# Kernel optimization log

Hardware: AMD Instinct MI355X
Metric: run time of the kernel (lower is better)

## Reference

```python
import jax, jax.numpy as jnp
import numpy as np
import math

B, T, D, NH, HS, NB = 1024, 64, 512, 8, 64, 225  # batch, squares, d_model, heads, head_size, buckets

def _displacement_buckets():
    sq = np.arange(T)
    rank, file = sq // 8, sq % 8
    d_rank = rank[None, :] - rank[:, None]
    d_file = file[None, :] - file[:, None]
    return jnp.asarray((d_rank + 7) * 15 + (d_file + 7))  # (64, 64) in [0, 225)

BUCKET = _displacement_buckets()

def setup_inputs() -> dict:
    key = jax.random.key(0)
    ks = jax.random.split(key, 6)
    return {
        "x": jax.random.normal(ks[0], (B, T, D), dtype=jnp.float32),
        "w_qkv": jax.random.normal(ks[1], (3 * D, D), dtype=jnp.float32) * 0.02,
        "w_proj": jax.random.normal(ks[2], (D, D), dtype=jnp.float32) * 0.02,
        "b_proj": jnp.zeros((D,), dtype=jnp.float32),
        "rel_k": jax.random.normal(ks[3], (NB, HS), dtype=jnp.float32) * 0.02,
        "rel_v": jax.random.normal(ks[4], (NB, HS), dtype=jnp.float32) * 0.02,
    }

def reference(x, w_qkv, w_proj, b_proj, rel_k, rel_v):
    b, t, d = x.shape
    qkv = x @ w_qkv.T                                   # (b, t, 3d)
    qkv = qkv.reshape(b, t, 3, NH, HS)                  # 'b t (three nh h)'
    q, k, v = jnp.moveaxis(qkv, 2, 0).transpose(0, 1, 3, 2, 4)  # each (b, nh, t, h)
    scale = 1.0 / math.sqrt(HS)
    rk = rel_k[BUCKET]                                  # (t, t, h)
    rv = rel_v[BUCKET]                                  # (t, t, h)
    logits = jnp.einsum('bhid,bhjd->bhij', q, k) + jnp.einsum('bhid,ijd->bhij', q, rk)
    attn = jax.nn.softmax(logits * scale, axis=-1)      # (b, nh, t, t)
    out = jnp.einsum('bhij,bhjd->bhid', attn, v) + jnp.einsum('bhij,ijd->bhid', attn, rv)
    out = out.transpose(0, 2, 1, 3).reshape(b, t, d)    # 'b nh t h -> b t (nh h)'
    return out @ w_proj.T + b_proj
```

## Files before the change

### kernel.cpp

```cpp
#include <hip/hip_runtime.h>
#include <hip/hip_bf16.h>
#include <stdint.h>
#include <stddef.h>

typedef __attribute__((ext_vector_type(8))) short bf16x8;
typedef __attribute__((ext_vector_type(4))) float f32x4;

typedef __attribute__((address_space(1))) const unsigned int g_as1;
typedef __attribute__((address_space(3))) unsigned int lds_as3;
__device__ __forceinline__ void gload_lds16(const void* g, void* l) {
  __builtin_amdgcn_global_load_lds((g_as1*)g, (lds_as3*)l, 16, 0, 0);
}

__device__ __forceinline__ unsigned short f2bf(float f) {
  union { float f; unsigned int u; } v; v.f = f;
  unsigned int u = v.u;
  u += 0x7fffu + ((u >> 16) & 1u);
  return (unsigned short)(u >> 16);
}
__device__ __forceinline__ float bf2f(unsigned short s) {
  union { unsigned int u; float f; } v; v.u = ((unsigned int)s) << 16;
  return v.f;
}
__device__ __forceinline__ unsigned cvt_pk_bf16(float lo, float hi) {
  __hip_bfloat162 h2 = __float22bfloat162_rn(make_float2(lo, hi));
  unsigned r;
  __builtin_memcpy(&r, &h2, 4);
  return r;
}


__global__ void prep_kernel(const float* __restrict__ wqkv,
                            const float* __restrict__ wproj,
                            const float* __restrict__ relk,
                            const float* __restrict__ relv,
                            short* __restrict__ wq_t,
                            short* __restrict__ wp_t,
                            short* __restrict__ relk_b,
                            short* __restrict__ relvT_b) {
  const int g = blockIdx.x * 256 + threadIdx.x;
  if (g < 98304) {
    const int row = g >> 6, c8 = g & 63;
    const float* s = wqkv + (size_t)row * 512 + c8 * 8;
    float4 f0 = *(const float4*)s;
    float4 f1 = *(const float4*)(s + 4);
    uint4 w;
    w.x = f2bf(f0.x) | ((unsigned)f2bf(f0.y) << 16);
    w.y = f2bf(f0.z) | ((unsigned)f2bf(f0.w) << 16);
    w.z = f2bf(f1.x) | ((unsigned)f2bf(f1.y) << 16);
    w.w = f2bf(f1.z) | ((unsigned)f2bf(f1.w) << 16);
    const int bn = row >> 7, rl = row & 127, kk = c8 >> 3, c8l = c8 & 7;
    char* d = (char*)wq_t + (size_t)(bn * 8 + kk) * 16384 + rl * 128 +
              ((c8l * 16) ^ ((rl & 7) << 4));
    *(uint4*)d = w;
  } else if (g < 131072) {
    const int g2 = g - 98304;
    const int row = g2 >> 6, c8 = g2 & 63;
    const float* s = wproj + (size_t)row * 512 + c8 * 8;
    float4 f0 = *(const float4*)s;
    float4 f1 = *(const float4*)(s + 4);
    uint4 w;
    w.x = f2bf(f0.x) | ((unsigned)f2bf(f0.y) << 16);
    w.y = f2bf(f0.z) | ((unsigned)f2bf(f0.w) << 16);
    w.z = f2bf(f1.x) | ((unsigned)f2bf(f1.y) << 16);
    w.w = f2bf(f1.z) | ((unsigned)f2bf(f1.w) << 16);
    const int bn = row >> 7, rl = row & 127, kk = c8 >> 3, c8l = c8 & 7;
    char* d = (char*)wp_t + (size_t)(bn * 8 + kk) * 16384 + rl * 128 +
              ((c8l * 16) ^ ((rl & 7) << 4));
    *(uint4*)d = w;
  } else if (g < 133120) {
    const int g3 = g - 131072;
    const int nb = g3 >> 3, c8 = g3 & 7;
    uint4 w = {0u, 0u, 0u, 0u};
    if (nb < 225) {
      const float* s = relk + (size_t)nb * 64 + c8 * 8;
      float4 f0 = *(const float4*)s;
      float4 f1 = *(const float4*)(s + 4);
      w.x = f2bf(f0.x) | ((unsigned)f2bf(f0.y) << 16);
      w.y = f2bf(f0.z) | ((unsigned)f2bf(f0.w) << 16);
      w.z = f2bf(f1.x) | ((unsigned)f2bf(f1.y) << 16);
      w.w = f2bf(f1.z) | ((unsigned)f2bf(f1.w) << 16);
    }
    *(uint4*)(relk_b + nb * 64 + c8 * 8) = w;
  } else {
    const int g4 = g - 133120;
    const int d = g4 >> 5, nb0 = (g4 & 31) * 8;
    unsigned short s[8];
#pragma unroll
    for (int j = 0; j < 8; ++j) {
      const int nb = nb0 + j;
      s[j] = (nb < 225) ? f2bf(relv[(size_t)nb * 64 + d]) : (unsigned short)0;
    }
    uint4 w;
    w.x = s[0] | ((unsigned)s[1] << 16);
    w.y = s[2] | ((unsigned)s[3] << 16);
    w.z = s[4] | ((unsigned)s[5] << 16);
    w.w = s[6] | ((unsigned)s[7] << 16);
    *(uint4*)(relvT_b + d * 256 + nb0) = w;
  }
}

__global__ void xconv_kernel(const float* __restrict__ x, short* __restrict__ x_t) {
  const int g = blockIdx.x * 256 + threadIdx.x;
  const int row = g >> 6, c8 = g & 63;
  const float* s = x + (size_t)row * 512 + c8 * 8;
  float4 f0 = *(const float4*)s;
  float4 f1 = *(const float4*)(s + 4);
  uint4 w;
  w.x = f2bf(f0.x) | ((unsigned)f2bf(f0.y) << 16);
  w.y = f2bf(f0.z) | ((unsigned)f2bf(f0.w) << 16);
  w.z = f2bf(f1.x) | ((unsigned)f2bf(f1.y) << 16);
  w.w = f2bf(f1.z) | ((unsigned)f2bf(f1.w) << 16);
  const int bm = row >> 7, rl = row & 127, kk = c8 >> 3, c8l = c8 & 7;
  char* d = (char*)x_t + (size_t)(bm * 8 + kk) * 16384 + rl * 128 +
            ((c8l * 16) ^ ((rl & 7) << 4));
  *(uint4*)d = w;
}

__global__ __launch_bounds__(256)
void qkv_gemm(const short* __restrict__ x_t, const short* __restrict__ wq_t,
              short* __restrict__ q_g, short* __restrict__ k_g,
              short* __restrict__ vT_g) {
  __shared__ __align__(16) short As[8192];
  __shared__ __align__(16) short Bs[8192];
  const int tid = threadIdx.x;
  const int lane = tid & 63;
  const int l15 = lane & 15, l4 = lane >> 4;
  const int wave = tid >> 6;
  const int wm = wave >> 1, wn = wave & 1;
  const int bid = blockIdx.x;
  const int wg = (bid & 7) * 768 + (bid >> 3);
  const int bn = wg % 12;
  const int bm = wg / 12;
  char* as_ = (char*)As;
  char* bs_ = (char*)Bs;
  const char* abase = (const char*)x_t + (size_t)bm * 131072;
  const char* bbase = (const char*)wq_t + (size_t)bn * 131072;
  const int soff = tid * 16;

  const f32x4 fz = {0.f, 0.f, 0.f, 0.f};
  f32x4 acc[4][4];
#pragma unroll
  for (int mt = 0; mt < 4; ++mt)
#pragma unroll
    for (int nt = 0; nt < 4; ++nt) acc[mt][nt] = fz;

#pragma unroll 1
  for (int kk = 0; kk < 8; ++kk) {
    const char* ga = abase + kk * 16384 + soff;
    const char* gb = bbase + kk * 16384 + soff;
#pragma unroll
    for (int i = 0; i < 4; ++i) {
      gload_lds16(ga + i * 4096, as_ + soff + i * 4096);
      gload_lds16(gb + i * 4096, bs_ + soff + i * 4096);
    }
    __syncthreads();
#pragma unroll
    for (int ki = 0; ki < 2; ++ki) {
      bf16x8 af[4], bfr[4];
#pragma unroll
      for (int mt = 0; mt < 4; ++mt) {
        const int row = 64 * wm + 16 * mt + l15;
        af[mt] = *(const bf16x8*)(as_ + row * 128 + ((64 * ki + 16 * l4) ^ ((row & 7) << 4)));
      }
#pragma unroll
      for (int nt = 0; nt < 4; ++nt) {
        const int row = 64 * wn + 16 * nt + l15;
        bfr[nt] = *(const bf16x8*)(bs_ + row * 128 + ((64 * ki + 16 * l4) ^ ((row & 7) << 4)));
      }
#pragma unroll
      for (int mt = 0; mt < 4; ++mt)
#pragma unroll
        for (int nt = 0; nt < 4; ++nt)
          acc[mt][nt] = __builtin_amdgcn_mfma_f32_16x16x32_bf16(af[mt], bfr[nt], acc[mt][nt], 0, 0, 0);
    }
    __syncthreads();
  }

  const int three = bn >> 2;
  if (three < 2) {
    short* dst = (three == 0) ? q_g : k_g;
#pragma unroll
    for (int mt = 0; mt < 4; ++mt) {
      const int m0 = bm * 128 + 64 * wm + 16 * mt + 4 * l4;
      const int b = m0 >> 6, t0 = m0 & 63;
#pragma unroll
      for (int nt = 0; nt < 4; ++nt) {
        const int n = bn * 128 + 64 * wn + 16 * nt + l15;
        const int h = (n >> 6) & 7, d = n & 63;
        short* p = dst + (size_t)(b * 8 + h) * 4096 + d;
#pragma unroll
        for (int jj = 0; jj < 4; ++jj)
          p[(t0 + jj) * 64] = (short)f2bf(acc[mt][nt][jj]);
      }
    }
  } else {
#pragma unroll
    for (int mt = 0; mt < 4; ++mt) {
      const int m0 = bm * 128 + 64 * wm + 16 * mt + 4 * l4;
      const int b = m0 >> 6, t0 = m0 & 63;
#pragma unroll
      for (int nt = 0; nt < 4; ++nt) {
        const int n = bn * 128 + 64 * wn + 16 * nt + l15;
        const int h = (n >> 6) & 7, d = n & 63;
        uint2 w;
        w.x = cvt_pk_bf16(acc[mt][nt][0], acc[mt][nt][1]);
        w.y = cvt_pk_bf16(acc[mt][nt][2], acc[mt][nt][3]);
        *(uint2*)(vT_g + (size_t)((b * 8 + h) * 64 + d) * 64 + t0) = w;
      }
    }
  }
}

__global__ __launch_bounds__(256, 4)
void attn_kernel(const short* __restrict__ q_g, const short* __restrict__ k_g,
                 const short* __restrict__ vT_g, const short* __restrict__ relk,
                 const short* __restrict__ relvT, short* __restrict__ aout_t) {
  __shared__ __align__(16) short srel_s[64 * 256];
  __shared__ __align__(16) short attn_s[64 * 64];
  const int tid = threadIdx.x, lane = tid & 63, w = tid >> 6;
  const int l15 = lane & 15, l4 = lane >> 4;
  const int bh = blockIdx.x;
  const short* qb = q_g + (size_t)bh * 4096;
  const short* kb = k_g + (size_t)bh * 4096;
  const short* vb = vT_g + (size_t)bh * 4096;
  char* ss = (char*)srel_s;
  char* as = (char*)attn_s;
  const f32x4 fz = {0.f, 0.f, 0.f, 0.f};

  bf16x8 bq[4][2];
#pragma unroll
  for (int nt = 0; nt < 4; ++nt)
#pragma unroll
    for (int kkk = 0; kkk < 2; ++kkk)
      bq[nt][kkk] = *(const bf16x8*)(qb + (16 * nt + l15) * 64 + 32 * kkk + 8 * l4);
#pragma unroll
  for (int mtl = 0; mtl < 4; ++mtl) {
    const int mt = 4 * w + mtl;
    bf16x8 ar0 = *(const bf16x8*)(relk + (16 * mt + l15) * 64 + 8 * l4);
    bf16x8 ar1 = *(const bf16x8*)(relk + (16 * mt + l15) * 64 + 32 + 8 * l4);
#pragma unroll
    for (int nt = 0; nt < 4; ++nt) {
      f32x4 a = fz;
      a = __builtin_amdgcn_mfma_f32_16x16x32_bf16(ar0, bq[nt][0], a, 0, 0, 0);
      a = __builtin_amdgcn_mfma_f32_16x16x32_bf16(ar1, bq[nt][1], a, 0, 0, 0);
      const int i = 16 * nt + l15;
      const int nb0 = 16 * mt + 4 * l4;
      uint2 wv;
      wv.x = cvt_pk_bf16(a[0], a[1]);
      wv.y = cvt_pk_bf16(a[2], a[3]);
      *(uint2*)(ss + i * 512 + ((nb0 * 2) ^ ((i & 7) << 4))) = wv;
    }
  }

  f32x4 sacc[4];
#pragma unroll
  for (int jt = 0; jt < 4; ++jt) {
    sacc[jt] = fz;
    bf16x8 ak0 = *(const bf16x8*)(kb + (16 * jt + l15) * 64 + 8 * l4);
    bf16x8 ak1 = *(const bf16x8*)(kb + (16 * jt + l15) * 64 + 32 + 8 * l4);
    sacc[jt] = __builtin_amdgcn_mfma_f32_16x16x32_bf16(ak0, bq[w][0], sacc[jt], 0, 0, 0);
    sacc[jt] = __builtin_amdgcn_mfma_f32_16x16x32_bf16(ak1, bq[w][1], sacc[jt], 0, 0, 0);
  }
  __syncthreads();

  const int i = 16 * w + l15;
  const int swz = (i & 7) << 4;
  const int ibase = i * 512;
  const int off2 = 2 * (15 * (l4 >> 1) + 4 * (l4 & 1) + 112 - (15 * (i >> 3) + (i & 7)));
  float p[16];
  float mx = -1e30f;
#pragma unroll
  for (int jt = 0; jt < 4; ++jt)
#pragma unroll
    for (int rg = 0; rg < 4; ++rg) {
      const int adr = ibase + (((60 * jt + 2 * rg) + off2) ^ swz);
      const float sr = bf2f(*(const unsigned short*)(ss + adr));
      const float lv = sacc[jt][rg] + sr;
      p[4 * jt + rg] = lv;
      mx = fmaxf(mx, lv);
    }
  mx = fmaxf(mx, __shfl_xor(mx, 16));
  mx = fmaxf(mx, __shfl_xor(mx, 32));
  float sum = 0.f;
#pragma unroll
  for (int q2 = 0; q2 < 16; ++q2) {
    p[q2] = __expf((p[q2] - mx) * 0.125f);
    sum += p[q2];
  }
  sum += __shfl_xor(sum, 16);
  sum += __shfl_xor(sum, 32);
  const float rs = 1.0f / sum;
  unsigned pk[8];
#pragma unroll
  for (int h2 = 0; h2 < 8; ++h2)
    pk[h2] = cvt_pk_bf16(p[2 * h2] * rs, p[2 * h2 + 1] * rs);
#pragma unroll
  for (int jt = 0; jt < 4; ++jt) {
    uint2 wv;
    wv.x = pk[2 * jt];
    wv.y = pk[2 * jt + 1];
    *(uint2*)(as + i * 128 + (((16 * jt + 4 * l4) * 2) ^ swz)) = wv;
  }
  {
    const uint4 uz = {0u, 0u, 0u, 0u};
#pragma unroll
    for (int c = 0; c < 8; ++c)
      *(uint4*)(ss + ibase + ((l4 * 128 + c * 16) ^ swz)) = uz;
  }
#pragma unroll
  for (int jt = 0; jt < 4; ++jt)
#pragma unroll
    for (int rg = 0; rg < 4; ++rg) {
      const int adr = ibase + (((60 * jt + 2 * rg) + off2) ^ swz);
      const int q2 = 4 * jt + rg;
      const unsigned v = pk[q2 >> 1] >> ((q2 & 1) * 16);
      *(unsigned short*)(ss + adr) = (unsigned short)v;
    }
  __syncthreads();

  f32x4 oacc[4];
#pragma unroll
  for (int nt = 0; nt < 4; ++nt) oacc[nt] = fz;
#pragma unroll
  for (int kkk = 0; kkk < 2; ++kkk) {
    bf16x8 av = *(const bf16x8*)(vb + (16 * w + l15) * 64 + 32 * kkk + 8 * l4);
#pragma unroll
    for (int nt = 0; nt < 4; ++nt) {
      const int t = 16 * nt + l15;
      bf16x8 bp = *(const bf16x8*)(as + t * 128 + (((32 * kkk + 8 * l4) * 2) ^ ((t & 7) << 4)));
      oacc[nt] = __builtin_amdgcn_mfma_f32_16x16x32_bf16(av, bp, oacc[nt], 0, 0, 0);
    }
  }
#pragma unroll
  for (int kkk = 0; kkk < 8; ++kkk) {
    bf16x8 arv = *(const bf16x8*)(relvT + (16 * w + l15) * 256 + 32 * kkk + 8 * l4);
#pragma unroll
    for (int nt = 0; nt < 4; ++nt) {
      const int t = 16 * nt + l15;
      bf16x8 bp = *(const bf16x8*)(ss + t * 512 + (((32 * kkk + 8 * l4) * 2) ^ ((t & 7) << 4)));
      oacc[nt] = __builtin_amdgcn_mfma_f32_16x16x32_bf16(arv, bp, oacc[nt], 0, 0, 0);
    }
  }
  const int b = bh >> 3, h = bh & 7;
  char* abase = (char*)aout_t + (size_t)((b >> 1) * 8 + h) * 16384;
  const int rbase = (b & 1) * 64;
#pragma unroll
  for (int nt = 0; nt < 4; ++nt) {
    const int t = 16 * nt + l15;
    const int r = rbase + t;
    const int d0 = 16 * w + 4 * l4;
    uint2 wv;
    wv.x = cvt_pk_bf16(oacc[nt][0], oacc[nt][1]);
    wv.y = cvt_pk_bf16(oacc[nt][2], oacc[nt][3]);
    *(uint2*)(abase + r * 128 + ((d0 * 2) ^ ((r & 7) << 4))) = wv;
  }
}

__global__ __launch_bounds__(256)
void proj_kernel(const short* __restrict__ a_t, const short* __restrict__ wp_t,
                 const float* __restrict__ bproj, float* __restrict__ out) {
  __shared__ __align__(16) short As[8192];
  __shared__ __align__(16) short Bs[8192];
  const int tid = threadIdx.x;
  const int lane = tid & 63;
  const int wave = tid >> 6;
  const int wm = wave >> 1, wn = wave & 1;
  const int l15 = lane & 15, l4 = lane >> 4;
  const int bid = blockIdx.x;
  const int wg = (bid & 7) * 256 + (bid >> 3);
  const int bn = wg & 3;
  const int bm = wg >> 2;
  char* as_ = (char*)As;
  char* bs_ = (char*)Bs;
  const char* abase = (const char*)a_t + (size_t)bm * 131072;
  const char* bbase = (const char*)wp_t + (size_t)bn * 131072;
  const int soff = tid * 16;

  const f32x4 fz = {0.f, 0.f, 0.f, 0.f};
  f32x4 acc[4][4];
#pragma unroll
  for (int mt = 0; mt < 4; ++mt)
#pragma unroll
    for (int nt = 0; nt < 4; ++nt) acc[mt][nt] = fz;

#pragma unroll 1
  for (int kk = 0; kk < 8; ++kk) {
    const char* ga = abase + kk * 16384 + soff;
    const char* gb = bbase + kk * 16384 + soff;
#pragma unroll
    for (int i = 0; i < 4; ++i) {
      gload_lds16(ga + i * 4096, as_ + soff + i * 4096);
      gload_lds16(gb + i * 4096, bs_ + soff + i * 4096);
    }
    __syncthreads();
#pragma unroll
    for (int ki = 0; ki < 2; ++ki) {
      bf16x8 af[4], bq[4];
#pragma unroll
      for (int mt = 0; mt < 4; ++mt) {
        const int row = 64 * wm + 16 * mt + l15;
        af[mt] = *(const bf16x8*)(as_ + row * 128 + ((64 * ki + 16 * l4) ^ ((row & 7) << 4)));
      }
#pragma unroll
      for (int nt = 0; nt < 4; ++nt) {
        const int row = 64 * wn + 16 * nt + l15;
        bq[nt] = *(const bf16x8*)(bs_ + row * 128 + ((64 * ki + 16 * l4) ^ ((row & 7) << 4)));
      }
#pragma unroll
      for (int mt = 0; mt < 4; ++mt)
#pragma unroll
        for (int nt = 0; nt < 4; ++nt)
          acc[mt][nt] = __builtin_amdgcn_mfma_f32_16x16x32_bf16(af[mt], bq[nt], acc[mt][nt], 0, 0, 0);
    }
    __syncthreads();
  }
#pragma unroll
  for (int nt = 0; nt < 4; ++nt) {
    const int col = bn * 128 + 64 * wn + 16 * nt + l15;
    const float bias = bproj[col];
#pragma unroll
    for (int mt = 0; mt < 4; ++mt) {
      const int r0 = bm * 128 + 64 * wm + 16 * mt + 4 * l4;
#pragma unroll
      for (int jj = 0; jj < 4; ++jj)
        out[(size_t)(r0 + jj) * 512 + col] = acc[mt][nt][jj] + bias;
    }
  }
}

extern "C" void kernel_launch(void* const* d_in, const int* in_sizes, int n_in,
                              void* d_out, int out_size, void* d_ws, size_t ws_size,
                              hipStream_t stream) {
  const float* x = (const float*)d_in[0];
  const float* wqkv = (const float*)d_in[1];
  const float* wproj = (const float*)d_in[2];
  const float* bproj = (const float*)d_in[3];
  const float* relk = (const float*)d_in[4];
  const float* relv = (const float*)d_in[5];
  float* out = (float*)d_out;

  char* ws = (char*)d_ws;
  const size_t MB = 1024 * 1024;
  short* xa_t = (short*)ws;
  short* vT_g = (short*)(ws + 64 * MB);
  short* wq_t = (short*)(ws + 128 * MB);
  short* wp_t = (short*)(ws + 128 * MB + 1572864);
  short* relk_b = (short*)(ws + 128 * MB + 2097152);
  short* relvT_b = (short*)(ws + 128 * MB + 2129920);
  short* q_gg = (short*)d_out;
  short* k_gg = (short*)((char*)d_out + 64 * MB);

  prep_kernel<<<dim3(528), dim3(256), 0, stream>>>(wqkv, wproj, relk, relv, wq_t,
                                                   wp_t, relk_b, relvT_b);
  xconv_kernel<<<dim3(16384), dim3(256), 0, stream>>>(x, xa_t);
  qkv_gemm<<<dim3(6144), dim3(256), 0, stream>>>(xa_t, wq_t, q_gg, k_gg, vT_g);
  attn_kernel<<<dim3(8192), dim3(256), 0, stream>>>(q_gg, k_gg, vT_g, relk_b,
                                                    relvT_b, xa_t);
  proj_kernel<<<dim3(2048), dim3(256), 0, stream>>>(xa_t, wp_t, bproj, out);
}
```

Baseline: 376.1 us.

## Use scaled FP8 MFMA for relative-value attention term and shrink LDS footprint

The attention-times-rel_v product now runs as an fp8 e4m3 MFMA instead of bf16. The scattered bucket probabilities are stored as scaled fp8 bytes in a half-size LDS buffer, and rel_v is pre-quantized to fp8 with a scale factor that is undone at output. LDS per block shrinks, so launch bounds are raised to 5 blocks per CU. V fragments are loaded early, and setprio hints are added around the MFMA sections, with an extra barrier before the buffer is reused. The change cuts LDS traffic and footprint and raises occupancy, at the cost of reduced precision in the rel_v contribution.

```diff
diff --git a/kernel.cpp b/kernel.cpp
--- a/kernel.cpp
+++ b/kernel.cpp
@@ -1,5 +1,6 @@
 #include <hip/hip_runtime.h>
 #include <hip/hip_bf16.h>
+#include <hip/hip_fp8.h>
 #include <stdint.h>
 #include <stddef.h>
 
@@ -27,6 +28,10 @@
   unsigned r;
   __builtin_memcpy(&r, &h2, 4);
   return r;
+}
+__device__ __forceinline__ unsigned char f2fp8(float f) {
+  __hip_fp8_e4m3 v(f);
+  return (unsigned char)v.__x;
 }
 
 
@@ -37,7 +42,7 @@
                             short* __restrict__ wq_t,
                             short* __restrict__ wp_t,
                             short* __restrict__ relk_b,
-                            short* __restrict__ relvT_b) {
+                            unsigned char* __restrict__ relv_f8) {
   const int g = blockIdx.x * 256 + threadIdx.x;
   if (g < 98304) {
     const int row = g >> 6, c8 = g & 63;
@@ -85,18 +90,15 @@
   } else {
     const int g4 = g - 133120;
     const int d = g4 >> 5, nb0 = (g4 & 31) * 8;
-    unsigned short s[8];
+    unsigned long long w8 = 0ull;
 #pragma unroll
     for (int j = 0; j < 8; ++j) {
       const int nb = nb0 + j;
-      s[j] = (nb < 225) ? f2bf(relv[(size_t)nb * 64 + d]) : (unsigned short)0;
-    }
-    uint4 w;
-    w.x = s[0] | ((unsigned)s[1] << 16);
-    w.y = s[2] | ((unsigned)s[3] << 16);
-    w.z = s[4] | ((unsigned)s[5] << 16);
-    w.w = s[6] | ((unsigned)s[7] << 16);
-    *(uint4*)(relvT_b + d * 256 + nb0) = w;
+      unsigned char b = 0;
+      if (nb < 225) b = f2fp8(relv[(size_t)nb * 64 + d] * 16.0f);
+      w8 |= ((unsigned long long)b) << (8 * j);
+    }
+    *(unsigned long long*)(relv_f8 + (size_t)d * 256 + nb0) = w8;
   }
 }
 
@@ -212,21 +214,23 @@
   }
 }
 
-__global__ __launch_bounds__(256, 4)
+__global__ __launch_bounds__(256, 5)
 void attn_kernel(const short* __restrict__ q_g, const short* __restrict__ k_g,
                  const short* __restrict__ vT_g, const short* __restrict__ relk,
-                 const short* __restrict__ relvT, short* __restrict__ aout_t) {
-  __shared__ __align__(16) short srel_s[64 * 256];
-  __shared__ __align__(16) short attn_s[64 * 64];
+                 const unsigned char* __restrict__ relv_f8,
+                 short* __restrict__ aout_t) {
+  __shared__ __align__(16) char ss[32768];
   const int tid = threadIdx.x, lane = tid & 63, w = tid >> 6;
   const int l15 = lane & 15, l4 = lane >> 4;
   const int bh = blockIdx.x;
   const short* qb = q_g + (size_t)bh * 4096;
   const short* kb = k_g + (size_t)bh * 4096;
   const short* vb = vT_g + (size_t)bh * 4096;
-  char* ss = (char*)srel_s;
-  char* as = (char*)attn_s;
+  char* as = ss + 16384;
   const f32x4 fz = {0.f, 0.f, 0.f, 0.f};
+
+  const bf16x8 av0 = *(const bf16x8*)(vb + (16 * w + l15) * 64 + 8 * l4);
+  const bf16x8 av1 = *(const bf16x8*)(vb + (16 * w + l15) * 64 + 32 + 8 * l4);
 
   bf16x8 bq[4][2];
 #pragma unroll
@@ -234,6 +238,7 @@
 #pragma unroll
     for (int kkk = 0; kkk < 2; ++kkk)
       bq[nt][kkk] = *(const bf16x8*)(qb + (16 * nt + l15) * 64 + 32 * kkk + 8 * l4);
+  __builtin_amdgcn_s_setprio(1);
 #pragma unroll
   for (int mtl = 0; mtl < 4; ++mtl) {
     const int mt = 4 * w + mtl;
@@ -262,12 +267,15 @@
     sacc[jt] = __builtin_amdgcn_mfma_f32_16x16x32_bf16(ak0, bq[w][0], sacc[jt], 0, 0, 0);
     sacc[jt] = __builtin_amdgcn_mfma_f32_16x16x32_bf16(ak1, bq[w][1], sacc[jt], 0, 0, 0);
   }
+  __builtin_amdgcn_s_setprio(0);
   __syncthreads();
 
   const int i = 16 * w + l15;
   const int swz = (i & 7) << 4;
+  const int swz8 = (i & 7) << 3;
   const int ibase = i * 512;
-  const int off2 = 2 * (15 * (l4 >> 1) + 4 * (l4 & 1) + 112 - (15 * (i >> 3) + (i & 7)));
+  const int off1 = 15 * (l4 >> 1) + 4 * (l4 & 1) + 112 - (15 * (i >> 3) + (i & 7));
+  const int off2 = 2 * off1;
   float p[16];
   float mx = -1e30f;
 #pragma unroll
@@ -291,10 +299,14 @@
   sum += __shfl_xor(sum, 16);
   sum += __shfl_xor(sum, 32);
   const float rs = 1.0f / sum;
+  const float rs64 = rs * 64.0f;
   unsigned pk[8];
 #pragma unroll
   for (int h2 = 0; h2 < 8; ++h2)
     pk[h2] = cvt_pk_bf16(p[2 * h2] * rs, p[2 * h2 + 1] * rs);
+
+  __syncthreads();
+
 #pragma unroll
   for (int jt = 0; jt < 4; ++jt) {
     uint2 wv;
@@ -305,54 +317,60 @@
   {
     const uint4 uz = {0u, 0u, 0u, 0u};
 #pragma unroll
-    for (int c = 0; c < 8; ++c)
-      *(uint4*)(ss + ibase + ((l4 * 128 + c * 16) ^ swz)) = uz;
+    for (int c = 0; c < 4; ++c)
+      *(uint4*)(ss + i * 256 + l4 * 64 + c * 16) = uz;
   }
 #pragma unroll
   for (int jt = 0; jt < 4; ++jt)
 #pragma unroll
     for (int rg = 0; rg < 4; ++rg) {
-      const int adr = ibase + (((60 * jt + 2 * rg) + off2) ^ swz);
-      const int q2 = 4 * jt + rg;
-      const unsigned v = pk[q2 >> 1] >> ((q2 & 1) * 16);
-      *(unsigned short*)(ss + adr) = (unsigned short)v;
+      const int nb = 30 * jt + rg + off1;
+      *(unsigned char*)(ss + i * 256 + (nb ^ swz8)) = f2fp8(p[4 * jt + rg] * rs64);
     }
   __syncthreads();
 
-  f32x4 oacc[4];
-#pragma unroll
-  for (int nt = 0; nt < 4; ++nt) oacc[nt] = fz;
+  f32x4 oq[4], orl[4];
+#pragma unroll
+  for (int nt = 0; nt < 4; ++nt) { oq[nt] = fz; orl[nt] = fz; }
+  __builtin_amdgcn_s_setprio(1);
 #pragma unroll
   for (int kkk = 0; kkk < 2; ++kkk) {
-    bf16x8 av = *(const bf16x8*)(vb + (16 * w + l15) * 64 + 32 * kkk + 8 * l4);
+    const bf16x8 av = kkk ? av1 : av0;
 #pragma unroll
     for (int nt = 0; nt < 4; ++nt) {
       const int t = 16 * nt + l15;
       bf16x8 bp = *(const bf16x8*)(as + t * 128 + (((32 * kkk + 8 * l4) * 2) ^ ((t & 7) << 4)));
-      oacc[nt] = __builtin_amdgcn_mfma_f32_16x16x32_bf16(av, bp, oacc[nt], 0, 0, 0);
+      oq[nt] = __builtin_amdgcn_mfma_f32_16x16x32_bf16(av, bp, oq[nt], 0, 0, 0);
     }
   }
 #pragma unroll
   for (int kkk = 0; kkk < 8; ++kkk) {
-    bf16x8 arv = *(const bf16x8*)(relvT + (16 * w + l15) * 256 + 32 * kkk + 8 * l4);
+    const long pa = *(const long*)(relv_f8 + (size_t)(16 * w + l15) * 256 + 32 * kkk + 8 * l4);
 #pragma unroll
     for (int nt = 0; nt < 4; ++nt) {
       const int t = 16 * nt + l15;
-      bf16x8 bp = *(const bf16x8*)(ss + t * 512 + (((32 * kkk + 8 * l4) * 2) ^ ((t & 7) << 4)));
-      oacc[nt] = __builtin_amdgcn_mfma_f32_16x16x32_bf16(arv, bp, oacc[nt], 0, 0, 0);
-    }
-  }
+      const long pb = *(const long*)(ss + t * 256 + ((32 * kkk + 8 * l4) ^ ((t & 7) << 3)));
+      orl[nt] = __builtin_amdgcn_mfma_f32_16x16x32_fp8_fp8(pa, pb, orl[nt], 0, 0, 0);
+    }
+  }
+  __builtin_amdgcn_s_setprio(0);
+
   const int b = bh >> 3, h = bh & 7;
   char* abase = (char*)aout_t + (size_t)((b >> 1) * 8 + h) * 16384;
   const int rbase = (b & 1) * 64;
+  const float rsc = 1.0f / 1024.0f;
 #pragma unroll
   for (int nt = 0; nt < 4; ++nt) {
     const int t = 16 * nt + l15;
     const int r = rbase + t;
     const int d0 = 16 * w + 4 * l4;
+    const float v0 = oq[nt][0] + orl[nt][0] * rsc;
+    const float v1 = oq[nt][1] + orl[nt][1] * rsc;
+    const float v2 = oq[nt][2] + orl[nt][2] * rsc;
+    const float v3 = oq[nt][3] + orl[nt][3] * rsc;
     uint2 wv;
-    wv.x = cvt_pk_bf16(oacc[nt][0], oacc[nt][1]);
-    wv.y = cvt_pk_bf16(oacc[nt][2], oacc[nt][3]);
+    wv.x = cvt_pk_bf16(v0, v1);
+    wv.y = cvt_pk_bf16(v2, v3);
     *(uint2*)(abase + r * 128 + ((d0 * 2) ^ ((r & 7) << 4))) = wv;
   }
 }
@@ -447,15 +465,15 @@
   short* wq_t = (short*)(ws + 128 * MB);
   short* wp_t = (short*)(ws + 128 * MB + 1572864);
   short* relk_b = (short*)(ws + 128 * MB + 2097152);
-  short* relvT_b = (short*)(ws + 128 * MB + 2129920);
+  unsigned char* relv_f8 = (unsigned char*)(ws + 128 * MB + 2129920);
   short* q_gg = (short*)d_out;
   short* k_gg = (short*)((char*)d_out + 64 * MB);
 
   prep_kernel<<<dim3(528), dim3(256), 0, stream>>>(wqkv, wproj, relk, relv, wq_t,
-                                                   wp_t, relk_b, relvT_b);
+                                                   wp_t, relk_b, relv_f8);
   xconv_kernel<<<dim3(16384), dim3(256), 0, stream>>>(x, xa_t);
   qkv_gemm<<<dim3(6144), dim3(256), 0, stream>>>(xa_t, wq_t, q_gg, k_gg, vT_g);
   attn_kernel<<<dim3(8192), dim3(256), 0, stream>>>(q_gg, k_gg, vT_g, relk_b,
-                                                    relvT_b, xa_t);
+                                                    relv_f8, xa_t);
   proj_kernel<<<dim3(2048), dim3(256), 0, stream>>>(xa_t, wp_t, bproj, out);
 }
```

Result: slower. 485.0 us (+28.9%).

## Swap PV operand roles so each wave consumes its own rows and drop barrier

Applied to the files above, without the earlier changes.

In the output stage the MFMA operands are swapped. Each wave now uses the attention and relative-probability rows it wrote itself as the A operand, with V and relvT streamed from global memory as the B operand. That makes the second __syncthreads between softmax and the PV matmuls unnecessary, so it is removed. The change also adds s_setprio around the MFMA phases and uses tree-shaped max and sum reductions in the softmax. The costs are 4x more global loads of relvT and V fragments, and output written as scattered 2-byte stores instead of 8-byte stores.

```diff
diff --git a/kernel.cpp b/kernel.cpp
--- a/kernel.cpp
+++ b/kernel.cpp
@@ -216,16 +216,14 @@
 void attn_kernel(const short* __restrict__ q_g, const short* __restrict__ k_g,
                  const short* __restrict__ vT_g, const short* __restrict__ relk,
                  const short* __restrict__ relvT, short* __restrict__ aout_t) {
-  __shared__ __align__(16) short srel_s[64 * 256];
-  __shared__ __align__(16) short attn_s[64 * 64];
+  __shared__ __align__(16) char ss[32768];
+  __shared__ __align__(16) char as[8192];
   const int tid = threadIdx.x, lane = tid & 63, w = tid >> 6;
   const int l15 = lane & 15, l4 = lane >> 4;
   const int bh = blockIdx.x;
   const short* qb = q_g + (size_t)bh * 4096;
   const short* kb = k_g + (size_t)bh * 4096;
   const short* vb = vT_g + (size_t)bh * 4096;
-  char* ss = (char*)srel_s;
-  char* as = (char*)attn_s;
   const f32x4 fz = {0.f, 0.f, 0.f, 0.f};
 
   bf16x8 bq[4][2];
@@ -234,6 +232,7 @@
 #pragma unroll
     for (int kkk = 0; kkk < 2; ++kkk)
       bq[nt][kkk] = *(const bf16x8*)(qb + (16 * nt + l15) * 64 + 32 * kkk + 8 * l4);
+  __builtin_amdgcn_s_setprio(1);
 #pragma unroll
   for (int mtl = 0; mtl < 4; ++mtl) {
     const int mt = 4 * w + mtl;
@@ -244,12 +243,12 @@
       f32x4 a = fz;
       a = __builtin_amdgcn_mfma_f32_16x16x32_bf16(ar0, bq[nt][0], a, 0, 0, 0);
       a = __builtin_amdgcn_mfma_f32_16x16x32_bf16(ar1, bq[nt][1], a, 0, 0, 0);
-      const int i = 16 * nt + l15;
+      const int ii = 16 * nt + l15;
       const int nb0 = 16 * mt + 4 * l4;
       uint2 wv;
       wv.x = cvt_pk_bf16(a[0], a[1]);
       wv.y = cvt_pk_bf16(a[2], a[3]);
-      *(uint2*)(ss + i * 512 + ((nb0 * 2) ^ ((i & 7) << 4))) = wv;
+      *(uint2*)(ss + ii * 512 + ((nb0 * 2) ^ ((ii & 7) << 4))) = wv;
     }
   }
 
@@ -262,6 +261,7 @@
     sacc[jt] = __builtin_amdgcn_mfma_f32_16x16x32_bf16(ak0, bq[w][0], sacc[jt], 0, 0, 0);
     sacc[jt] = __builtin_amdgcn_mfma_f32_16x16x32_bf16(ak1, bq[w][1], sacc[jt], 0, 0, 0);
   }
+  __builtin_amdgcn_s_setprio(0);
   __syncthreads();
 
   const int i = 16 * w + l15;
@@ -269,25 +269,30 @@
   const int ibase = i * 512;
   const int off2 = 2 * (15 * (l4 >> 1) + 4 * (l4 & 1) + 112 - (15 * (i >> 3) + (i & 7)));
   float p[16];
-  float mx = -1e30f;
 #pragma unroll
   for (int jt = 0; jt < 4; ++jt)
 #pragma unroll
     for (int rg = 0; rg < 4; ++rg) {
       const int adr = ibase + (((60 * jt + 2 * rg) + off2) ^ swz);
       const float sr = bf2f(*(const unsigned short*)(ss + adr));
-      const float lv = sacc[jt][rg] + sr;
-      p[4 * jt + rg] = lv;
-      mx = fmaxf(mx, lv);
-    }
+      p[4 * jt + rg] = sacc[jt][rg] + sr;
+    }
+  float m8[8], m4[4];
+#pragma unroll
+  for (int h2 = 0; h2 < 8; ++h2) m8[h2] = fmaxf(p[2 * h2], p[2 * h2 + 1]);
+#pragma unroll
+  for (int h2 = 0; h2 < 4; ++h2) m4[h2] = fmaxf(m8[2 * h2], m8[2 * h2 + 1]);
+  float mx = fmaxf(fmaxf(m4[0], m4[1]), fmaxf(m4[2], m4[3]));
   mx = fmaxf(mx, __shfl_xor(mx, 16));
   mx = fmaxf(mx, __shfl_xor(mx, 32));
-  float sum = 0.f;
-#pragma unroll
-  for (int q2 = 0; q2 < 16; ++q2) {
-    p[q2] = __expf((p[q2] - mx) * 0.125f);
-    sum += p[q2];
-  }
+#pragma unroll
+  for (int q2 = 0; q2 < 16; ++q2) p[q2] = __expf((p[q2] - mx) * 0.125f);
+  float s8[8], s4[4];
+#pragma unroll
+  for (int h2 = 0; h2 < 8; ++h2) s8[h2] = p[2 * h2] + p[2 * h2 + 1];
+#pragma unroll
+  for (int h2 = 0; h2 < 4; ++h2) s4[h2] = s8[2 * h2] + s8[2 * h2 + 1];
+  float sum = (s4[0] + s4[1]) + (s4[2] + s4[3]);
   sum += __shfl_xor(sum, 16);
   sum += __shfl_xor(sum, 32);
   const float rs = 1.0f / sum;
@@ -295,6 +300,7 @@
 #pragma unroll
   for (int h2 = 0; h2 < 8; ++h2)
     pk[h2] = cvt_pk_bf16(p[2 * h2] * rs, p[2 * h2 + 1] * rs);
+
 #pragma unroll
   for (int jt = 0; jt < 4; ++jt) {
     uint2 wv;
@@ -317,43 +323,45 @@
       const unsigned v = pk[q2 >> 1] >> ((q2 & 1) * 16);
       *(unsigned short*)(ss + adr) = (unsigned short)v;
     }
-  __syncthreads();
 
   f32x4 oacc[4];
 #pragma unroll
-  for (int nt = 0; nt < 4; ++nt) oacc[nt] = fz;
-#pragma unroll
-  for (int kkk = 0; kkk < 2; ++kkk) {
-    bf16x8 av = *(const bf16x8*)(vb + (16 * w + l15) * 64 + 32 * kkk + 8 * l4);
-#pragma unroll
-    for (int nt = 0; nt < 4; ++nt) {
-      const int t = 16 * nt + l15;
-      bf16x8 bp = *(const bf16x8*)(as + t * 128 + (((32 * kkk + 8 * l4) * 2) ^ ((t & 7) << 4)));
-      oacc[nt] = __builtin_amdgcn_mfma_f32_16x16x32_bf16(av, bp, oacc[nt], 0, 0, 0);
-    }
-  }
-#pragma unroll
-  for (int kkk = 0; kkk < 8; ++kkk) {
-    bf16x8 arv = *(const bf16x8*)(relvT + (16 * w + l15) * 256 + 32 * kkk + 8 * l4);
-#pragma unroll
-    for (int nt = 0; nt < 4; ++nt) {
-      const int t = 16 * nt + l15;
-      bf16x8 bp = *(const bf16x8*)(ss + t * 512 + (((32 * kkk + 8 * l4) * 2) ^ ((t & 7) << 4)));
-      oacc[nt] = __builtin_amdgcn_mfma_f32_16x16x32_bf16(arv, bp, oacc[nt], 0, 0, 0);
-    }
-  }
+  for (int dt = 0; dt < 4; ++dt) oacc[dt] = fz;
+  __builtin_amdgcn_s_setprio(1);
+#pragma unroll
+  for (int kk = 0; kk < 2; ++kk) {
+    bf16x8 aA = *(const bf16x8*)(as + i * 128 + (((32 * kk + 8 * l4) * 2) ^ swz));
+#pragma unroll
+    for (int dt = 0; dt < 4; ++dt) {
+      bf16x8 bV = *(const bf16x8*)(vb + (16 * dt + l15) * 64 + 32 * kk + 8 * l4);
+      oacc[dt] = __builtin_amdgcn_mfma_f32_16x16x32_bf16(aA, bV, oacc[dt], 0, 0, 0);
+    }
+  }
+#pragma unroll
+  for (int kk = 0; kk < 8; ++kk) {
+    bf16x8 aP = *(const bf16x8*)(ss + ibase + (((32 * kk + 8 * l4) * 2) ^ swz));
+#pragma unroll
+    for (int dt = 0; dt < 4; ++dt) {
+      bf16x8 bR = *(const bf16x8*)(relvT + (16 * dt + l15) * 256 + 32 * kk + 8 * l4);
+      oacc[dt] = __builtin_amdgcn_mfma_f32_16x16x32_bf16(aP, bR, oacc[dt], 0, 0, 0);
+    }
+  }
+  __builtin_amdgcn_s_setprio(0);
+
   const int b = bh >> 3, h = bh & 7;
   char* abase = (char*)aout_t + (size_t)((b >> 1) * 8 + h) * 16384;
   const int rbase = (b & 1) * 64;
 #pragma unroll
-  for (int nt = 0; nt < 4; ++nt) {
-    const int t = 16 * nt + l15;
-    const int r = rbase + t;
-    const int d0 = 16 * w + 4 * l4;
-    uint2 wv;
-    wv.x = cvt_pk_bf16(oacc[nt][0], oacc[nt][1]);
-    wv.y = cvt_pk_bf16(oacc[nt][2], oacc[nt][3]);
-    *(uint2*)(abase + r * 128 + ((d0 * 2) ^ ((r & 7) << 4))) = wv;
+  for (int dt = 0; dt < 4; ++dt) {
+    const unsigned pkA = cvt_pk_bf16(oacc[dt][0], oacc[dt][1]);
+    const unsigned pkB = cvt_pk_bf16(oacc[dt][2], oacc[dt][3]);
+    const int d2 = 2 * (16 * dt + l15);
+#pragma unroll
+    for (int jj = 0; jj < 4; ++jj) {
+      const int r = rbase + 16 * w + 4 * l4 + jj;
+      const unsigned v = (jj < 2) ? (pkA >> (16 * (jj & 1))) : (pkB >> (16 * (jj & 1)));
+      *(unsigned short*)(abase + r * 128 + (d2 ^ ((r & 7) << 4))) = (unsigned short)v;
+    }
   }
 }
 
```

New measurement: 488.0 us. 29.7% more time.

## Fuse fp32-to-bf16 conversion of x into QKV GEMM and raise MFMA priority

Applied to the files above, without the earlier changes.

Removes the separate xconv kernel. The QKV GEMM now loads fp32 x tiles into registers, converts them to bf16 and writes them swizzled into LDS, prefetching the next k-slice while the current one is consumed. This avoids a full bf16 write and re-read of x (64 MB), at the cost of each of the 12 N-blocks re-reading fp32 x from memory or cache. It also wraps the MFMA sections of the attention kernel in s_setprio raises so matrix work is favoured across waves.

```diff
diff --git a/kernel.cpp b/kernel.cpp
--- a/kernel.cpp
+++ b/kernel.cpp
@@ -100,25 +100,8 @@
   }
 }
 
-__global__ void xconv_kernel(const float* __restrict__ x, short* __restrict__ x_t) {
-  const int g = blockIdx.x * 256 + threadIdx.x;
-  const int row = g >> 6, c8 = g & 63;
-  const float* s = x + (size_t)row * 512 + c8 * 8;
-  float4 f0 = *(const float4*)s;
-  float4 f1 = *(const float4*)(s + 4);
-  uint4 w;
-  w.x = f2bf(f0.x) | ((unsigned)f2bf(f0.y) << 16);
-  w.y = f2bf(f0.z) | ((unsigned)f2bf(f0.w) << 16);
-  w.z = f2bf(f1.x) | ((unsigned)f2bf(f1.y) << 16);
-  w.w = f2bf(f1.z) | ((unsigned)f2bf(f1.w) << 16);
-  const int bm = row >> 7, rl = row & 127, kk = c8 >> 3, c8l = c8 & 7;
-  char* d = (char*)x_t + (size_t)(bm * 8 + kk) * 16384 + rl * 128 +
-            ((c8l * 16) ^ ((rl & 7) << 4));
-  *(uint4*)d = w;
-}
-
 __global__ __launch_bounds__(256)
-void qkv_gemm(const short* __restrict__ x_t, const short* __restrict__ wq_t,
+void qkv_gemm(const float* __restrict__ x, const short* __restrict__ wq_t,
               short* __restrict__ q_g, short* __restrict__ k_g,
               short* __restrict__ vT_g) {
   __shared__ __align__(16) short As[8192];
@@ -134,10 +117,20 @@
   const int bm = wg / 12;
   char* as_ = (char*)As;
   char* bs_ = (char*)Bs;
-  const char* abase = (const char*)x_t + (size_t)bm * 131072;
   const char* bbase = (const char*)wq_t + (size_t)bn * 131072;
   const int soff = tid * 16;
 
+  int arow[4], ac8[4], adst[4];
+  const float* asrc[4];
+#pragma unroll
+  for (int r = 0; r < 4; ++r) {
+    const int gid = r * 256 + tid;
+    arow[r] = gid >> 3;
+    ac8[r] = gid & 7;
+    adst[r] = arow[r] * 128 + ((ac8[r] * 16) ^ ((arow[r] & 7) << 4));
+    asrc[r] = x + (size_t)(bm * 128 + arow[r]) * 512 + ac8[r] * 8;
+  }
+
   const f32x4 fz = {0.f, 0.f, 0.f, 0.f};
   f32x4 acc[4][4];
 #pragma unroll
@@ -145,14 +138,34 @@
 #pragma unroll
     for (int nt = 0; nt < 4; ++nt) acc[mt][nt] = fz;
 
+  float4 fa[4][2];
+#pragma unroll
+  for (int r = 0; r < 4; ++r) {
+    fa[r][0] = *(const float4*)(asrc[r]);
+    fa[r][1] = *(const float4*)(asrc[r] + 4);
+  }
+
 #pragma unroll 1
   for (int kk = 0; kk < 8; ++kk) {
-    const char* ga = abase + kk * 16384 + soff;
     const char* gb = bbase + kk * 16384 + soff;
 #pragma unroll
-    for (int i = 0; i < 4; ++i) {
-      gload_lds16(ga + i * 4096, as_ + soff + i * 4096);
+    for (int i = 0; i < 4; ++i)
       gload_lds16(gb + i * 4096, bs_ + soff + i * 4096);
+#pragma unroll
+    for (int r = 0; r < 4; ++r) {
+      uint4 w;
+      w.x = cvt_pk_bf16(fa[r][0].x, fa[r][0].y);
+      w.y = cvt_pk_bf16(fa[r][0].z, fa[r][0].w);
+      w.z = cvt_pk_bf16(fa[r][1].x, fa[r][1].y);
+      w.w = cvt_pk_bf16(fa[r][1].z, fa[r][1].w);
+      *(uint4*)(as_ + adst[r]) = w;
+    }
+    if (kk < 7) {
+#pragma unroll
+      for (int r = 0; r < 4; ++r) {
+        fa[r][0] = *(const float4*)(asrc[r] + (kk + 1) * 64);
+        fa[r][1] = *(const float4*)(asrc[r] + (kk + 1) * 64 + 4);
+      }
     }
     __syncthreads();
 #pragma unroll
@@ -234,6 +247,7 @@
 #pragma unroll
     for (int kkk = 0; kkk < 2; ++kkk)
       bq[nt][kkk] = *(const bf16x8*)(qb + (16 * nt + l15) * 64 + 32 * kkk + 8 * l4);
+  __builtin_amdgcn_s_setprio(1);
 #pragma unroll
   for (int mtl = 0; mtl < 4; ++mtl) {
     const int mt = 4 * w + mtl;
@@ -262,6 +276,7 @@
     sacc[jt] = __builtin_amdgcn_mfma_f32_16x16x32_bf16(ak0, bq[w][0], sacc[jt], 0, 0, 0);
     sacc[jt] = __builtin_amdgcn_mfma_f32_16x16x32_bf16(ak1, bq[w][1], sacc[jt], 0, 0, 0);
   }
+  __builtin_amdgcn_s_setprio(0);
   __syncthreads();
 
   const int i = 16 * w + l15;
@@ -322,6 +337,7 @@
   f32x4 oacc[4];
 #pragma unroll
   for (int nt = 0; nt < 4; ++nt) oacc[nt] = fz;
+  __builtin_amdgcn_s_setprio(1);
 #pragma unroll
   for (int kkk = 0; kkk < 2; ++kkk) {
     bf16x8 av = *(const bf16x8*)(vb + (16 * w + l15) * 64 + 32 * kkk + 8 * l4);
@@ -342,6 +358,8 @@
       oacc[nt] = __builtin_amdgcn_mfma_f32_16x16x32_bf16(arv, bp, oacc[nt], 0, 0, 0);
     }
   }
+  __builtin_amdgcn_s_setprio(0);
+
   const int b = bh >> 3, h = bh & 7;
   char* abase = (char*)aout_t + (size_t)((b >> 1) * 8 + h) * 16384;
   const int rbase = (b & 1) * 64;
@@ -442,7 +460,7 @@
 
   char* ws = (char*)d_ws;
   const size_t MB = 1024 * 1024;
-  short* xa_t = (short*)ws;
+  short* aout_t = (short*)ws;
   short* vT_g = (short*)(ws + 64 * MB);
   short* wq_t = (short*)(ws + 128 * MB);
   short* wp_t = (short*)(ws + 128 * MB + 1572864);
@@ -453,9 +471,8 @@
 
   prep_kernel<<<dim3(528), dim3(256), 0, stream>>>(wqkv, wproj, relk, relv, wq_t,
                                                    wp_t, relk_b, relvT_b);
-  xconv_kernel<<<dim3(16384), dim3(256), 0, stream>>>(x, xa_t);
-  qkv_gemm<<<dim3(6144), dim3(256), 0, stream>>>(xa_t, wq_t, q_gg, k_gg, vT_g);
+  qkv_gemm<<<dim3(6144), dim3(256), 0, stream>>>(x, wq_t, q_gg, k_gg, vT_g);
   attn_kernel<<<dim3(8192), dim3(256), 0, stream>>>(q_gg, k_gg, vT_g, relk_b,
-                                                    relvT_b, xa_t);
-  proj_kernel<<<dim3(2048), dim3(256), 0, stream>>>(xa_t, wp_t, bproj, out);
-}
+                                                    relvT_b, aout_t);
+  proj_kernel<<<dim3(2048), dim3(256), 0, stream>>>(aout_t, wp_t, bproj, out);
+}
```

After: 410.9 us. 1.09x slower.
